# Kernel optimization log

Hardware: AMD Instinct MI355X
Metric: run time of the kernel (lower is better)

## Reference

```python
import jax, jax.numpy as jnp
import numpy as np

N = 50000      # nodes
E = 1_600_000  # edges (avg degree 32)
INP, HID, OUT = 256, 512, 256
N_REST = 11    # GCNConv layers beyond the first (12 total)
BN_EPS = 1e-5


def setup_inputs() -> dict:
    key = jax.random.key(0)
    ks = jax.random.split(key, 8)
    s = 0.05
    return {
        "x": jax.random.normal(ks[0], (N, INP), jnp.float32),
        "edge_index": jax.random.randint(ks[1], (2, E), 0, N, dtype=jnp.int64),
        "W_first": jax.random.normal(ks[2], (INP, HID), jnp.float32) * s,
        "b_first": jnp.zeros((HID,), jnp.float32),
        "W_rest": jax.random.normal(ks[3], (N_REST, HID, HID), jnp.float32) * s,
        "b_rest": jnp.zeros((N_REST, HID), jnp.float32),
        "bn_gamma": jnp.ones((2, HID), jnp.float32),
        "bn_beta": jnp.zeros((2, HID), jnp.float32),
        "out_W": jax.random.normal(ks[4], (HID, OUT), jnp.float32) * s,
        "out_b": jnp.zeros((OUT,), jnp.float32),
    }


def _gelu(v):
    return jax.nn.gelu(v, approximate=False)  # nn.GELU default (erf)


def reference(x, edge_index, W_first, b_first, W_rest, b_rest,
              bn_gamma, bn_beta, out_W, out_b):
    n = x.shape[0]
    # GCN normalization with self-loops: A_hat = D^-1/2 (A + I) D^-1/2
    loops = jnp.arange(n, dtype=edge_index.dtype)
    row = jnp.concatenate([edge_index[0], loops])  # source
    col = jnp.concatenate([edge_index[1], loops])  # target
    deg = jax.ops.segment_sum(jnp.ones_like(col, x.dtype), col, num_segments=n)
    dinv = jnp.where(deg > 0, jax.lax.rsqrt(deg), 0.0)
    norm = dinv[row] * dinv[col]  # [E+N]

    def conv(h, W, b):
        msg = (h @ W)[row] * norm[:, None]                      # gather + scale
        return jax.ops.segment_sum(msg, col, num_segments=n) + b  # scatter-add

    def bn(h, g, bta):  # BatchNorm1d, training-mode batch stats
        mu = h.mean(0)
        var = h.var(0)
        return (h - mu) * jax.lax.rsqrt(var + BN_EPS) * g + bta

    # block 0: conv, gelu, conv, gelu, conv (pyg BasicGNN: no act after last)
    h = conv(x, W_first, b_first)
    h = conv(_gelu(h), W_rest[0], b_rest[0])
    h = conv(_gelu(h), W_rest[1], b_rest[1])
    wi = 2
    for blk in range(3):
        h = conv(h, W_rest[wi], b_rest[wi])
        h = conv(_gelu(h), W_rest[wi + 1], b_rest[wi + 1])
        h = conv(_gelu(h), W_rest[wi + 2], b_rest[wi + 2])
        wi += 3
        if blk != 2:
            h = _gelu(bn(h, bn_gamma[blk], bn_beta[blk]))
    return h @ out_W + out_b
```

## Files before the change

### kernel.cpp

```cpp
#include <hip/hip_runtime.h>
#include <hip/hip_fp16.h>
#include <math.h>

#define INP 256
#define HID 512
#define OUTD 256

typedef _Float16 f16x8 __attribute__((ext_vector_type(8)));
typedef float f32x4 __attribute__((ext_vector_type(4)));

__device__ __forceinline__ float gelu_f(float x) {
  return 0.5f * x * (1.0f + erff(x * 0.7071067811865475f));
}

__device__ __forceinline__ void fma4(float4& a, float w, const float4& x) {
  a.x = fmaf(w, x.x, a.x);
  a.y = fmaf(w, x.y, a.y);
  a.z = fmaf(w, x.z, a.z);
  a.w = fmaf(w, x.w, a.w);
}

__device__ __forceinline__ void fma8h(float4& a0, float4& a1, float w,
                                      const float4& rv) {
  const __half2* h = (const __half2*)&rv;
  float2 f0 = __half22float2(h[0]);
  float2 f1 = __half22float2(h[1]);
  float2 f2 = __half22float2(h[2]);
  float2 f3 = __half22float2(h[3]);
  a0.x = fmaf(w, f0.x, a0.x); a0.y = fmaf(w, f0.y, a0.y);
  a0.z = fmaf(w, f1.x, a0.z); a0.w = fmaf(w, f1.y, a0.w);
  a1.x = fmaf(w, f2.x, a1.x); a1.y = fmaf(w, f2.y, a1.y);
  a1.z = fmaf(w, f3.x, a1.z); a1.w = fmaf(w, f3.y, a1.w);
}


__global__ void hist_k(const int* __restrict__ col, int* __restrict__ cnt, int E) {
  int e = blockIdx.x * blockDim.x + threadIdx.x;
  if (e < E) atomicAdd(&cnt[col[e]], 1);
}

__global__ void dinv_k(const int* __restrict__ cnt, float* __restrict__ dinv, int n) {
  int i = blockIdx.x * blockDim.x + threadIdx.x;
  if (i < n) dinv[i] = rsqrtf((float)(cnt[i] + 1));
}

__global__ void scan1_k(const int* __restrict__ cnt, int* __restrict__ offs,
                        int* __restrict__ bsum, int n) {
  __shared__ int s[256];
  int t = threadIdx.x;
  int i = blockIdx.x * 256 + t;
  int v = (i < n) ? cnt[i] : 0;
  s[t] = v;
  __syncthreads();
  #pragma unroll
  for (int off = 1; off < 256; off <<= 1) {
    int u = (t >= off) ? s[t - off] : 0;
    __syncthreads();
    s[t] += u;
    __syncthreads();
  }
  if (i < n) offs[i] = s[t] - v;
  if (t == 255) bsum[blockIdx.x] = s[255];
}

__global__ void scan2_k(int* __restrict__ bsum, int nb) {
  __shared__ int s[256];
  int t = threadIdx.x;
  int v = (t < nb) ? bsum[t] : 0;
  s[t] = v;
  __syncthreads();
  #pragma unroll
  for (int off = 1; off < 256; off <<= 1) {
    int u = (t >= off) ? s[t - off] : 0;
    __syncthreads();
    s[t] += u;
    __syncthreads();
  }
  if (t < nb) bsum[t] = s[t] - v;
}

__global__ void scan3_k(int* __restrict__ offs, const int* __restrict__ bsum, int n) {
  int i = blockIdx.x * 256 + threadIdx.x;
  if (i < n) offs[i] += bsum[blockIdx.x];
}

__global__ void scatter_k(const int* __restrict__ row, const int* __restrict__ col,
                          const int* __restrict__ offs, int* __restrict__ cur,
                          const float* __restrict__ dinv, int* __restrict__ srcs,
                          float* __restrict__ norms, int E) {
  int e = blockIdx.x * blockDim.x + threadIdx.x;
  if (e >= E) return;
  int r = row[e], c = col[e];
  int p = offs[c] + atomicAdd(&cur[c], 1);
  srcs[p] = r;
  norms[p] = dinv[r] * dinv[c];
}

template <int PRO, int BIAS, int HALFC>
__global__ __launch_bounds__(256) void gemm_k(
    const float* __restrict__ A, const float* __restrict__ B, void* __restrict__ Cv,
    int M, int K, int NN, const float* __restrict__ bias,
    const float* __restrict__ scale, const float* __restrict__ shift) {
  __shared__ f16x8 Asl[4][128];
  __shared__ f16x8 Bsl[4][128];
  const int t = threadIdx.x;
  const int l = t & 63, wid = t >> 6;
  const int lid = l & 15, cc = l >> 4;
  const int wr = wid >> 1, wc = wid & 1;
  const int bm = blockIdx.x * 128, bn = blockIdx.y * 128;

  const int aq = t & 3;
  const int am = t >> 2;
  const int bc = t >> 6;
  const int bn0 = t & 63;

  f32x4 acc[4][4];
  #pragma unroll
  for (int i = 0; i < 4; ++i)
    #pragma unroll
    for (int j = 0; j < 4; ++j) acc[i][j] = (f32x4)0.f;

  for (int k0 = 0; k0 < K; k0 += 32) {
    #pragma unroll
    for (int h = 0; h < 2; ++h) {
      const int m = am + h * 64;
      const int gm = bm + m;
      const int gk = k0 + aq * 8;
      float4 v0 = make_float4(0.f, 0.f, 0.f, 0.f), v1 = v0;
      if (gm < M) {
        v0 = *(const float4*)(A + (size_t)gm * K + gk);
        v1 = *(const float4*)(A + (size_t)gm * K + gk + 4);
      }
      if (PRO == 2) {
        const float4 s0 = *(const float4*)(scale + gk);
        const float4 s1 = *(const float4*)(scale + gk + 4);
        const float4 h0 = *(const float4*)(shift + gk);
        const float4 h1 = *(const float4*)(shift + gk + 4);
        v0.x = fmaf(v0.x, s0.x, h0.x); v0.y = fmaf(v0.y, s0.y, h0.y);
        v0.z = fmaf(v0.z, s0.z, h0.z); v0.w = fmaf(v0.w, s0.w, h0.w);
        v1.x = fmaf(v1.x, s1.x, h1.x); v1.y = fmaf(v1.y, s1.y, h1.y);
        v1.z = fmaf(v1.z, s1.z, h1.z); v1.w = fmaf(v1.w, s1.w, h1.w);
      }
      if (PRO >= 1) {
        v0.x = gelu_f(v0.x); v0.y = gelu_f(v0.y);
        v0.z = gelu_f(v0.z); v0.w = gelu_f(v0.w);
        v1.x = gelu_f(v1.x); v1.y = gelu_f(v1.y);
        v1.z = gelu_f(v1.z); v1.w = gelu_f(v1.w);
      }
      f16x8 hv;
      hv[0] = (_Float16)v0.x; hv[1] = (_Float16)v0.y;
      hv[2] = (_Float16)v0.z; hv[3] = (_Float16)v0.w;
      hv[4] = (_Float16)v1.x; hv[5] = (_Float16)v1.y;
      hv[6] = (_Float16)v1.z; hv[7] = (_Float16)v1.w;
      Asl[aq][m] = hv;
    }
    #pragma unroll
    for (int h = 0; h < 2; ++h) {
      const int nn = bn0 + h * 64;
      f16x8 hv;
      #pragma unroll
      for (int j = 0; j < 8; ++j)
        hv[j] = (_Float16)B[(size_t)(k0 + bc * 8 + j) * NN + bn + nn];
      Bsl[bc][nn] = hv;
    }
    __syncthreads();
    f16x8 af[4], bf[4];
    #pragma unroll
    for (int i = 0; i < 4; ++i) af[i] = Asl[cc][wr * 64 + i * 16 + lid];
    #pragma unroll
    for (int j = 0; j < 4; ++j) bf[j] = Bsl[cc][wc * 64 + j * 16 + lid];
    #pragma unroll
    for (int i = 0; i < 4; ++i)
      #pragma unroll
      for (int j = 0; j < 4; ++j)
        acc[i][j] = __builtin_amdgcn_mfma_f32_16x16x32_f16(af[i], bf[j],
                                                           acc[i][j], 0, 0, 0);
    __syncthreads();
  }

  #pragma unroll
  for (int j = 0; j < 4; ++j) {
    const int col = bn + wc * 64 + j * 16 + lid;
    const float bv = BIAS ? bias[col] : 0.f;
    #pragma unroll
    for (int i = 0; i < 4; ++i) {
      #pragma unroll
      for (int r = 0; r < 4; ++r) {
        const int row = bm + wr * 64 + i * 16 + cc * 4 + r;
        if (row < M) {
          const float o = acc[i][j][r] + bv;
          if (HALFC)
            ((__half*)Cv)[(size_t)row * NN + col] = __float2half(o);
          else
            ((float*)Cv)[(size_t)row * NN + col] = o;
        }
      }
    }
  }
}

template <int D>
__global__ __launch_bounds__(256) void agg_k(
    const float* __restrict__ xw, const int* __restrict__ srcs,
    const float* __restrict__ norms, const int* __restrict__ offs,
    const int* __restrict__ cnt, const float* __restrict__ dinv,
    const float* __restrict__ bias, float* __restrict__ out, int n) {
  constexpr int NV = D / 256;
  int wid = (blockIdx.x * blockDim.x + threadIdx.x) >> 6;
  int lane = threadIdx.x & 63;
  if (wid >= n) return;
  const int base = offs[wid];
  const int num = cnt[wid];

  float4 acc[NV];
  #pragma unroll
  for (int v = 0; v < NV; ++v) acc[v] = make_float4(0.f, 0.f, 0.f, 0.f);

  int sA[4], sB[4];
  float wA[4], wB[4];
  float4 rA[4][NV], rB[4][NV];

  auto ldidx = [&](int e, int& s, float& w) {
    bool ok = e < num;
    s = ok ? srcs[base + e] : 0;
    w = ok ? norms[base + e] : 0.f;
  };

  const int nw = (num + 3) >> 2;

  if (nw > 0) {
    #pragma unroll
    for (int j = 0; j < 4; ++j) ldidx(j, sA[j], wA[j]);
    #pragma unroll
    for (int j = 0; j < 4; ++j) {
      const float4* rp = (const float4*)(xw + (size_t)sA[j] * D);
      #pragma unroll
      for (int v = 0; v < NV; ++v) rA[j][v] = rp[v * 64 + lane];
    }
    int w = 0;
    for (; w + 2 <= nw; w += 2) {
      #pragma unroll
      for (int j = 0; j < 4; ++j) ldidx((w + 1) * 4 + j, sB[j], wB[j]);
      #pragma unroll
      for (int j = 0; j < 4; ++j) {
        const float4* rp = (const float4*)(xw + (size_t)sB[j] * D);
        #pragma unroll
        for (int v = 0; v < NV; ++v) rB[j][v] = rp[v * 64 + lane];
      }
      #pragma unroll
      for (int j = 0; j < 4; ++j)
        #pragma unroll
        for (int v = 0; v < NV; ++v) fma4(acc[v], wA[j], rA[j][v]);
      if (w + 2 < nw) {
        #pragma unroll
        for (int j = 0; j < 4; ++j) ldidx((w + 2) * 4 + j, sA[j], wA[j]);
        #pragma unroll
        for (int j = 0; j < 4; ++j) {
          const float4* rp = (const float4*)(xw + (size_t)sA[j] * D);
          #pragma unroll
          for (int v = 0; v < NV; ++v) rA[j][v] = rp[v * 64 + lane];
        }
      }
      #pragma unroll
      for (int j = 0; j < 4; ++j)
        #pragma unroll
        for (int v = 0; v < NV; ++v) fma4(acc[v], wB[j], rB[j][v]);
    }
    if (w < nw) {
      #pragma unroll
      for (int j = 0; j < 4; ++j)
        #pragma unroll
        for (int v = 0; v < NV; ++v) fma4(acc[v], wA[j], rA[j][v]);
    }
  }

  {
    float di = dinv[wid];
    float ws = di * di;
    const float4* rs = (const float4*)(xw + (size_t)wid * D);
    #pragma unroll
    for (int v = 0; v < NV; ++v) {
      float4 xs = rs[v * 64 + lane];
      fma4(acc[v], ws, xs);
    }
  }
  if (bias) {
    #pragma unroll
    for (int v = 0; v < NV; ++v) {
      float4 b = ((const float4*)bias)[v * 64 + lane];
      acc[v].x += b.x; acc[v].y += b.y; acc[v].z += b.z; acc[v].w += b.w;
    }
  }
  float4* op = (float4*)(out + (size_t)wid * D);
  #pragma unroll
  for (int v = 0; v < NV; ++v) op[v * 64 + lane] = acc[v];
}

__global__ __launch_bounds__(256) void agg_h_k(
    const __half* __restrict__ xwh, const int* __restrict__ srcs,
    const float* __restrict__ norms, const int* __restrict__ offs,
    const int* __restrict__ cnt, const float* __restrict__ dinv,
    const float* __restrict__ bias, float* __restrict__ out, int n) {
  int wid = (blockIdx.x * blockDim.x + threadIdx.x) >> 6;
  int lane = threadIdx.x & 63;
  if (wid >= n) return;
  const int base = offs[wid];
  const int num = cnt[wid];

  float4 a0 = make_float4(0.f, 0.f, 0.f, 0.f);
  float4 a1 = make_float4(0.f, 0.f, 0.f, 0.f);

  int sA[4], sB[4];
  float wA[4], wB[4];
  float4 rA[4], rB[4];

  auto ldidx = [&](int e, int& s, float& w) {
    bool ok = e < num;
    s = ok ? srcs[base + e] : 0;
    w = ok ? norms[base + e] : 0.f;
  };

  const int nw = (num + 3) >> 2;

  if (nw > 0) {
    #pragma unroll
    for (int j = 0; j < 4; ++j) ldidx(j, sA[j], wA[j]);
    #pragma unroll
    for (int j = 0; j < 4; ++j)
      rA[j] = ((const float4*)(xwh + (size_t)sA[j] * HID))[lane];
    int w = 0;
    for (; w + 2 <= nw; w += 2) {
      #pragma unroll
      for (int j = 0; j < 4; ++j) ldidx((w + 1) * 4 + j, sB[j], wB[j]);
      #pragma unroll
      for (int j = 0; j < 4; ++j)
        rB[j] = ((const float4*)(xwh + (size_t)sB[j] * HID))[lane];
      #pragma unroll
      for (int j = 0; j < 4; ++j) fma8h(a0, a1, wA[j], rA[j]);
      if (w + 2 < nw) {
        #pragma unroll
        for (int j = 0; j < 4; ++j) ldidx((w + 2) * 4 + j, sA[j], wA[j]);
        #pragma unroll
        for (int j = 0; j < 4; ++j)
          rA[j] = ((const float4*)(xwh + (size_t)sA[j] * HID))[lane];
      }
      #pragma unroll
      for (int j = 0; j < 4; ++j) fma8h(a0, a1, wB[j], rB[j]);
    }
    if (w < nw) {
      #pragma unroll
      for (int j = 0; j < 4; ++j) fma8h(a0, a1, wA[j], rA[j]);
    }
  }

  {
    float di = dinv[wid];
    float ws = di * di;
    float4 rs = ((const float4*)(xwh + (size_t)wid * HID))[lane];
    fma8h(a0, a1, ws, rs);
  }
  const float4 b0 = *(const float4*)(bias + lane * 8);
  const float4 b1 = *(const float4*)(bias + lane * 8 + 4);
  a0.x += b0.x; a0.y += b0.y; a0.z += b0.z; a0.w += b0.w;
  a1.x += b1.x; a1.y += b1.y; a1.z += b1.z; a1.w += b1.w;
  float* op = out + (size_t)wid * HID + lane * 8;
  *(float4*)op = a0;
  *(float4*)(op + 4) = a1;
}

__global__ __launch_bounds__(512) void bn_stats_k(const float* __restrict__ F,
                                                  float* __restrict__ sums, int n) {
  int t = threadIdx.x;
  int r0 = blockIdx.x * 128;
  int r1 = min(r0 + 128, n);
  float s = 0.f, s2 = 0.f;
  for (int r = r0; r < r1; ++r) {
    float v = F[(size_t)r * HID + t];
    s += v;
    s2 = fmaf(v, v, s2);
  }
  atomicAdd(&sums[t], s);
  atomicAdd(&sums[HID + t], s2);
}

__global__ void bn_fin_k(const float* __restrict__ sums, const float* __restrict__ g,
                         const float* __restrict__ b, float* __restrict__ scale,
                         float* __restrict__ shift, int n) {
  int t = threadIdx.x;
  float inv = 1.0f / (float)n;
  float mu = sums[t] * inv;
  float var = fmaf(-mu, mu, sums[HID + t] * inv);
  float rs = rsqrtf(var + 1e-5f);
  float sc = g[t] * rs;
  scale[t] = sc;
  shift[t] = fmaf(-mu, sc, b[t]);
}

extern "C" void kernel_launch(void* const* d_in, const int* in_sizes, int n_in,
                              void* d_out, int out_size, void* d_ws, size_t ws_size,
                              hipStream_t stream) {
  const float* x     = (const float*)d_in[0];
  const int*   ei    = (const int*)d_in[1];
  const float* Wf    = (const float*)d_in[2];
  const float* bf    = (const float*)d_in[3];
  const float* Wr    = (const float*)d_in[4];
  const float* br    = (const float*)d_in[5];
  const float* gamma = (const float*)d_in[6];
  const float* beta  = (const float*)d_in[7];
  const float* Wo    = (const float*)d_in[8];
  const float* bo    = (const float*)d_in[9];
  float* out = (float*)d_out;

  const int n = in_sizes[0] / INP;
  const int E = in_sizes[1] / 2;
  const int* erow = ei;
  const int* ecol = ei + E;

  char* w = (char*)d_ws;
  float*  f0   = (float*)w;  w += (size_t)n * HID * sizeof(float);
  __half* xwh  = (__half*)w; w += (size_t)n * HID * sizeof(__half);
  float*  t256 = (float*)w;  w += (size_t)n * INP * sizeof(float);

  char* q = (char*)d_out;
  int*   srcs  = (int*)q;   q += (size_t)E * sizeof(int);
  float* norms = (float*)q; q += (size_t)E * sizeof(float);
  int*   cnt   = (int*)q;   q += (size_t)n * sizeof(int);
  int*   cur   = (int*)q;   q += (size_t)n * sizeof(int);
  int*   offs  = (int*)q;   q += (size_t)n * sizeof(int);
  int*   bsum  = (int*)q;   q += 256 * sizeof(int);
  float* dinv  = (float*)q; q += (size_t)n * sizeof(float);
  float* bnsum = (float*)q; q += 1024 * sizeof(float);
  float* bnsc  = (float*)q; q += 512 * sizeof(float);
  float* bnsh  = (float*)q; q += 512 * sizeof(float);

  hipMemsetAsync(cnt, 0, (size_t)n * sizeof(int), stream);
  hipMemsetAsync(cur, 0, (size_t)n * sizeof(int), stream);

  const int eb = (E + 255) / 256;
  const int nb = (n + 255) / 256;
  hist_k<<<eb, 256, 0, stream>>>(ecol, cnt, E);
  dinv_k<<<nb, 256, 0, stream>>>(cnt, dinv, n);
  scan1_k<<<nb, 256, 0, stream>>>(cnt, offs, bsum, n);
  scan2_k<<<1, 256, 0, stream>>>(bsum, nb);
  scan3_k<<<nb, 256, 0, stream>>>(offs, bsum, n);
  scatter_k<<<eb, 256, 0, stream>>>(erow, ecol, offs, cur, dinv, srcs, norms, E);

  const dim3 blk(256);
  const int mg = (n + 127) / 128;
  const dim3 g512(mg, HID / 128);
  const dim3 g256(mg, OUTD / 128);
  const int aggBlocks = (n + 3) / 4;

  auto conv = [&](const float* W, const float* b, int pro) {
    if (pro == 1)
      gemm_k<1, 0, 1><<<g512, blk, 0, stream>>>(f0, W, xwh, n, HID, HID, nullptr, nullptr, nullptr);
    else if (pro == 2)
      gemm_k<2, 0, 1><<<g512, blk, 0, stream>>>(f0, W, xwh, n, HID, HID, nullptr, bnsc, bnsh);
    else
      gemm_k<0, 0, 1><<<g512, blk, 0, stream>>>(f0, W, xwh, n, HID, HID, nullptr, nullptr, nullptr);
    agg_h_k<<<aggBlocks, blk, 0, stream>>>(xwh, srcs, norms, offs, cnt, dinv, b, f0, n);
  };
  auto bn = [&](const float* F, int g) {
    hipMemsetAsync(bnsum, 0, 1024 * sizeof(float), stream);
    bn_stats_k<<<(n + 127) / 128, 512, 0, stream>>>(F, bnsum, n);
    bn_fin_k<<<1, 512, 0, stream>>>(bnsum, gamma + (size_t)g * HID,
                                    beta + (size_t)g * HID, bnsc, bnsh, n);
  };
  const size_t WS = (size_t)HID * HID;

  agg_k<INP><<<aggBlocks, blk, 0, stream>>>(x, srcs, norms, offs, cnt, dinv,
                                            nullptr, t256, n);
  gemm_k<0, 1, 0><<<g512, blk, 0, stream>>>(t256, Wf, f0, n, INP, HID, bf, nullptr, nullptr);

  conv(Wr + 0 * WS,  br + 0 * HID,  1);
  conv(Wr + 1 * WS,  br + 1 * HID,  1);
  conv(Wr + 2 * WS,  br + 2 * HID,  0);
  conv(Wr + 3 * WS,  br + 3 * HID,  1);
  conv(Wr + 4 * WS,  br + 4 * HID,  1);
  bn(f0, 0);
  conv(Wr + 5 * WS,  br + 5 * HID,  2);
  conv(Wr + 6 * WS,  br + 6 * HID,  1);
  conv(Wr + 7 * WS,  br + 7 * HID,  1);
  bn(f0, 1);
  conv(Wr + 8 * WS,  br + 8 * HID,  2);
  conv(Wr + 9 * WS,  br + 9 * HID,  1);
  conv(Wr + 10 * WS, br + 10 * HID, 1);
  gemm_k<0, 1, 0><<<g256, blk, 0, stream>>>(f0, Wo, out, n, HID, OUTD, bo, nullptr, nullptr);
}
```

Baseline: 4.550 ms.

## Store inter-layer activations in fp16 and move GELU into producer epilogues

Activations between layers are now stored as fp16 instead of fp32. The input x is cast to fp16 up front, the first aggregation reads fp16 rows, and GELU is applied once in the aggregation or GEMM epilogue rather than in every GEMM tile's prologue. This roughly halves the bytes moved by GEMM A-loads, aggregation writes and BN stats, and stops GELU being recomputed for each column tile. In exchange it adds a cast kernel and extra fp16 rounding of activations, and BN statistics are computed from fp16 values.

```diff
diff --git a/kernel.cpp b/kernel.cpp
--- a/kernel.cpp
+++ b/kernel.cpp
@@ -7,17 +7,11 @@
 #define OUTD 256
 
 typedef _Float16 f16x8 __attribute__((ext_vector_type(8)));
+typedef _Float16 f16x4 __attribute__((ext_vector_type(4)));
 typedef float f32x4 __attribute__((ext_vector_type(4)));
 
 __device__ __forceinline__ float gelu_f(float x) {
   return 0.5f * x * (1.0f + erff(x * 0.7071067811865475f));
-}
-
-__device__ __forceinline__ void fma4(float4& a, float w, const float4& x) {
-  a.x = fmaf(w, x.x, a.x);
-  a.y = fmaf(w, x.y, a.y);
-  a.z = fmaf(w, x.z, a.z);
-  a.w = fmaf(w, x.w, a.w);
 }
 
 __device__ __forceinline__ void fma8h(float4& a0, float4& a1, float w,
@@ -33,6 +27,29 @@
   a1.z = fmaf(w, f3.x, a1.z); a1.w = fmaf(w, f3.y, a1.w);
 }
 
+__device__ __forceinline__ void fma4h(float4& a, float w, const float2& rv) {
+  const __half2* h = (const __half2*)&rv;
+  float2 f0 = __half22float2(h[0]);
+  float2 f1 = __half22float2(h[1]);
+  a.x = fmaf(w, f0.x, a.x); a.y = fmaf(w, f0.y, a.y);
+  a.z = fmaf(w, f1.x, a.z); a.w = fmaf(w, f1.y, a.w);
+}
+
+
+__global__ void cast16_k(const float* __restrict__ in, __half* __restrict__ o,
+                         int nElem) {
+  int i = (blockIdx.x * blockDim.x + threadIdx.x) * 8;
+  if (i >= nElem) return;
+  float4 v0 = *(const float4*)(in + i);
+  float4 v1 = *(const float4*)(in + i + 4);
+  f16x8 hv;
+  hv[0] = (_Float16)v0.x; hv[1] = (_Float16)v0.y;
+  hv[2] = (_Float16)v0.z; hv[3] = (_Float16)v0.w;
+  hv[4] = (_Float16)v1.x; hv[5] = (_Float16)v1.y;
+  hv[6] = (_Float16)v1.z; hv[7] = (_Float16)v1.w;
+  *(f16x8*)(o + i) = hv;
+}
+
 
 __global__ void hist_k(const int* __restrict__ col, int* __restrict__ cnt, int E) {
   int e = blockIdx.x * blockDim.x + threadIdx.x;
@@ -96,9 +113,9 @@
   norms[p] = dinv[r] * dinv[c];
 }
 
-template <int PRO, int BIAS, int HALFC>
+template <int PRO, int BIAS, int HALFC, int EPI>
 __global__ __launch_bounds__(256) void gemm_k(
-    const float* __restrict__ A, const float* __restrict__ B, void* __restrict__ Cv,
+    const __half* __restrict__ A, const float* __restrict__ B, void* __restrict__ Cv,
     int M, int K, int NN, const float* __restrict__ bias,
     const float* __restrict__ scale, const float* __restrict__ shift) {
   __shared__ f16x8 Asl[4][128];
@@ -126,32 +143,23 @@
       const int m = am + h * 64;
       const int gm = bm + m;
       const int gk = k0 + aq * 8;
-      float4 v0 = make_float4(0.f, 0.f, 0.f, 0.f), v1 = v0;
-      if (gm < M) {
-        v0 = *(const float4*)(A + (size_t)gm * K + gk);
-        v1 = *(const float4*)(A + (size_t)gm * K + gk + 4);
-      }
+      f16x8 hv;
+      if (gm < M) hv = *(const f16x8*)(A + (size_t)gm * K + gk);
+      else hv = (f16x8)(_Float16)0;
       if (PRO == 2) {
         const float4 s0 = *(const float4*)(scale + gk);
         const float4 s1 = *(const float4*)(scale + gk + 4);
         const float4 h0 = *(const float4*)(shift + gk);
         const float4 h1 = *(const float4*)(shift + gk + 4);
-        v0.x = fmaf(v0.x, s0.x, h0.x); v0.y = fmaf(v0.y, s0.y, h0.y);
-        v0.z = fmaf(v0.z, s0.z, h0.z); v0.w = fmaf(v0.w, s0.w, h0.w);
-        v1.x = fmaf(v1.x, s1.x, h1.x); v1.y = fmaf(v1.y, s1.y, h1.y);
-        v1.z = fmaf(v1.z, s1.z, h1.z); v1.w = fmaf(v1.w, s1.w, h1.w);
+        const float sc[8] = {s0.x, s0.y, s0.z, s0.w, s1.x, s1.y, s1.z, s1.w};
+        const float sh[8] = {h0.x, h0.y, h0.z, h0.w, h1.x, h1.y, h1.z, h1.w};
+        #pragma unroll
+        for (int j = 0; j < 8; ++j) {
+          float v = (float)hv[j];
+          v = gelu_f(fmaf(v, sc[j], sh[j]));
+          hv[j] = (_Float16)v;
+        }
       }
-      if (PRO >= 1) {
-        v0.x = gelu_f(v0.x); v0.y = gelu_f(v0.y);
-        v0.z = gelu_f(v0.z); v0.w = gelu_f(v0.w);
-        v1.x = gelu_f(v1.x); v1.y = gelu_f(v1.y);
-        v1.z = gelu_f(v1.z); v1.w = gelu_f(v1.w);
-      }
-      f16x8 hv;
-      hv[0] = (_Float16)v0.x; hv[1] = (_Float16)v0.y;
-      hv[2] = (_Float16)v0.z; hv[3] = (_Float16)v0.w;
-      hv[4] = (_Float16)v1.x; hv[5] = (_Float16)v1.y;
-      hv[6] = (_Float16)v1.z; hv[7] = (_Float16)v1.w;
       Asl[aq][m] = hv;
     }
     #pragma unroll
@@ -188,7 +196,8 @@
       for (int r = 0; r < 4; ++r) {
         const int row = bm + wr * 64 + i * 16 + cc * 4 + r;
         if (row < M) {
-          const float o = acc[i][j][r] + bv;
+          float o = acc[i][j][r] + bv;
+          if (EPI) o = gelu_f(o);
           if (HALFC)
             ((__half*)Cv)[(size_t)row * NN + col] = __float2half(o);
           else
@@ -199,108 +208,12 @@
   }
 }
 
-template <int D>
-__global__ __launch_bounds__(256) void agg_k(
-    const float* __restrict__ xw, const int* __restrict__ srcs,
-    const float* __restrict__ norms, const int* __restrict__ offs,
-    const int* __restrict__ cnt, const float* __restrict__ dinv,
-    const float* __restrict__ bias, float* __restrict__ out, int n) {
-  constexpr int NV = D / 256;
-  int wid = (blockIdx.x * blockDim.x + threadIdx.x) >> 6;
-  int lane = threadIdx.x & 63;
-  if (wid >= n) return;
-  const int base = offs[wid];
-  const int num = cnt[wid];
-
-  float4 acc[NV];
-  #pragma unroll
-  for (int v = 0; v < NV; ++v) acc[v] = make_float4(0.f, 0.f, 0.f, 0.f);
-
-  int sA[4], sB[4];
-  float wA[4], wB[4];
-  float4 rA[4][NV], rB[4][NV];
-
-  auto ldidx = [&](int e, int& s, float& w) {
-    bool ok = e < num;
-    s = ok ? srcs[base + e] : 0;
-    w = ok ? norms[base + e] : 0.f;
-  };
-
-  const int nw = (num + 3) >> 2;
-
-  if (nw > 0) {
-    #pragma unroll
-    for (int j = 0; j < 4; ++j) ldidx(j, sA[j], wA[j]);
-    #pragma unroll
-    for (int j = 0; j < 4; ++j) {
-      const float4* rp = (const float4*)(xw + (size_t)sA[j] * D);
-      #pragma unroll
-      for (int v = 0; v < NV; ++v) rA[j][v] = rp[v * 64 + lane];
-    }
-    int w = 0;
-    for (; w + 2 <= nw; w += 2) {
-      #pragma unroll
-      for (int j = 0; j < 4; ++j) ldidx((w + 1) * 4 + j, sB[j], wB[j]);
-      #pragma unroll
-      for (int j = 0; j < 4; ++j) {
-        const float4* rp = (const float4*)(xw + (size_t)sB[j] * D);
-        #pragma unroll
-        for (int v = 0; v < NV; ++v) rB[j][v] = rp[v * 64 + lane];
-      }
-      #pragma unroll
-      for (int j = 0; j < 4; ++j)
-        #pragma unroll
-        for (int v = 0; v < NV; ++v) fma4(acc[v], wA[j], rA[j][v]);
-      if (w + 2 < nw) {
-        #pragma unroll
-        for (int j = 0; j < 4; ++j) ldidx((w + 2) * 4 + j, sA[j], wA[j]);
-        #pragma unroll
-        for (int j = 0; j < 4; ++j) {
-          const float4* rp = (const float4*)(xw + (size_t)sA[j] * D);
-          #pragma unroll
-          for (int v = 0; v < NV; ++v) rA[j][v] = rp[v * 64 + lane];
-        }
-      }
-      #pragma unroll
-      for (int j = 0; j < 4; ++j)
-        #pragma unroll
-        for (int v = 0; v < NV; ++v) fma4(acc[v], wB[j], rB[j][v]);
-    }
-    if (w < nw) {
-      #pragma unroll
-      for (int j = 0; j < 4; ++j)
-        #pragma unroll
-        for (int v = 0; v < NV; ++v) fma4(acc[v], wA[j], rA[j][v]);
-    }
-  }
-
-  {
-    float di = dinv[wid];
-    float ws = di * di;
-    const float4* rs = (const float4*)(xw + (size_t)wid * D);
-    #pragma unroll
-    for (int v = 0; v < NV; ++v) {
-      float4 xs = rs[v * 64 + lane];
-      fma4(acc[v], ws, xs);
-    }
-  }
-  if (bias) {
-    #pragma unroll
-    for (int v = 0; v < NV; ++v) {
-      float4 b = ((const float4*)bias)[v * 64 + lane];
-      acc[v].x += b.x; acc[v].y += b.y; acc[v].z += b.z; acc[v].w += b.w;
-    }
-  }
-  float4* op = (float4*)(out + (size_t)wid * D);
-  #pragma unroll
-  for (int v = 0; v < NV; ++v) op[v * 64 + lane] = acc[v];
-}
-
-__global__ __launch_bounds__(256) void agg_h_k(
+template <int EPI>
+__global__ __launch_bounds__(256) void agg512_k(
     const __half* __restrict__ xwh, const int* __restrict__ srcs,
     const float* __restrict__ norms, const int* __restrict__ offs,
     const int* __restrict__ cnt, const float* __restrict__ dinv,
-    const float* __restrict__ bias, float* __restrict__ out, int n) {
+    const float* __restrict__ bias, __half* __restrict__ out, int n) {
   int wid = (blockIdx.x * blockDim.x + threadIdx.x) >> 6;
   int lane = threadIdx.x & 63;
   if (wid >= n) return;
@@ -361,21 +274,93 @@
   }
   const float4 b0 = *(const float4*)(bias + lane * 8);
   const float4 b1 = *(const float4*)(bias + lane * 8 + 4);
-  a0.x += b0.x; a0.y += b0.y; a0.z += b0.z; a0.w += b0.w;
-  a1.x += b1.x; a1.y += b1.y; a1.z += b1.z; a1.w += b1.w;
-  float* op = out + (size_t)wid * HID + lane * 8;
-  *(float4*)op = a0;
-  *(float4*)(op + 4) = a1;
-}
-
-__global__ __launch_bounds__(512) void bn_stats_k(const float* __restrict__ F,
-                                                  float* __restrict__ sums, int n) {
+  float o[8] = {a0.x + b0.x, a0.y + b0.y, a0.z + b0.z, a0.w + b0.w,
+                a1.x + b1.x, a1.y + b1.y, a1.z + b1.z, a1.w + b1.w};
+  f16x8 hv;
+  #pragma unroll
+  for (int j = 0; j < 8; ++j) {
+    float v = EPI ? gelu_f(o[j]) : o[j];
+    hv[j] = (_Float16)v;
+  }
+  *(f16x8*)(out + (size_t)wid * HID + lane * 8) = hv;
+}
+
+__global__ __launch_bounds__(256) void agg256_k(
+    const __half* __restrict__ x16, const int* __restrict__ srcs,
+    const float* __restrict__ norms, const int* __restrict__ offs,
+    const int* __restrict__ cnt, const float* __restrict__ dinv,
+    __half* __restrict__ out, int n) {
+  int wid = (blockIdx.x * blockDim.x + threadIdx.x) >> 6;
+  int lane = threadIdx.x & 63;
+  if (wid >= n) return;
+  const int base = offs[wid];
+  const int num = cnt[wid];
+
+  float4 a0 = make_float4(0.f, 0.f, 0.f, 0.f);
+
+  int sA[4], sB[4];
+  float wA[4], wB[4];
+  float2 rA[4], rB[4];
+
+  auto ldidx = [&](int e, int& s, float& w) {
+    bool ok = e < num;
+    s = ok ? srcs[base + e] : 0;
+    w = ok ? norms[base + e] : 0.f;
+  };
+
+  const int nw = (num + 3) >> 2;
+
+  if (nw > 0) {
+    #pragma unroll
+    for (int j = 0; j < 4; ++j) ldidx(j, sA[j], wA[j]);
+    #pragma unroll
+    for (int j = 0; j < 4; ++j)
+      rA[j] = ((const float2*)(x16 + (size_t)sA[j] * INP))[lane];
+    int w = 0;
+    for (; w + 2 <= nw; w += 2) {
+      #pragma unroll
+      for (int j = 0; j < 4; ++j) ldidx((w + 1) * 4 + j, sB[j], wB[j]);
+      #pragma unroll
+      for (int j = 0; j < 4; ++j)
+        rB[j] = ((const float2*)(x16 + (size_t)sB[j] * INP))[lane];
+      #pragma unroll
+      for (int j = 0; j < 4; ++j) fma4h(a0, wA[j], rA[j]);
+      if (w + 2 < nw) {
+        #pragma unroll
+        for (int j = 0; j < 4; ++j) ldidx((w + 2) * 4 + j, sA[j], wA[j]);
+        #pragma unroll
+        for (int j = 0; j < 4; ++j)
+          rA[j] = ((const float2*)(x16 + (size_t)sA[j] * INP))[lane];
+      }
+      #pragma unroll
+      for (int j = 0; j < 4; ++j) fma4h(a0, wB[j], rB[j]);
+    }
+    if (w < nw) {
+      #pragma unroll
+      for (int j = 0; j < 4; ++j) fma4h(a0, wA[j], rA[j]);
+    }
+  }
+
+  {
+    float di = dinv[wid];
+    float ws = di * di;
+    float2 rs = ((const float2*)(x16 + (size_t)wid * INP))[lane];
+    fma4h(a0, ws, rs);
+  }
+  f16x4 hv;
+  hv[0] = (_Float16)a0.x; hv[1] = (_Float16)a0.y;
+  hv[2] = (_Float16)a0.z; hv[3] = (_Float16)a0.w;
+  *(f16x4*)(out + (size_t)wid * INP + lane * 4) = hv;
+}
+
+__global__ __launch_bounds__(512) void bn_stats_h_k(const __half* __restrict__ F,
+                                                    float* __restrict__ sums, int n) {
   int t = threadIdx.x;
   int r0 = blockIdx.x * 128;
   int r1 = min(r0 + 128, n);
   float s = 0.f, s2 = 0.f;
   for (int r = r0; r < r1; ++r) {
-    float v = F[(size_t)r * HID + t];
+    float v = __half2float(F[(size_t)r * HID + t]);
     s += v;
     s2 = fmaf(v, v, s2);
   }
@@ -417,9 +402,10 @@
   const int* ecol = ei + E;
 
   char* w = (char*)d_ws;
-  float*  f0   = (float*)w;  w += (size_t)n * HID * sizeof(float);
-  __half* xwh  = (__half*)w; w += (size_t)n * HID * sizeof(__half);
-  float*  t256 = (float*)w;  w += (size_t)n * INP * sizeof(float);
+  __half* a16   = (__half*)w; w += (size_t)n * HID * sizeof(__half);
+  __half* xwh   = (__half*)w; w += (size_t)n * HID * sizeof(__half);
+  __half* x16   = (__half*)w; w += (size_t)n * INP * sizeof(__half);
+  __half* t256h = (__half*)w; w += (size_t)n * INP * sizeof(__half);
 
   char* q = (char*)d_out;
   int*   srcs  = (int*)q;   q += (size_t)E * sizeof(int);
@@ -438,6 +424,7 @@
 
   const int eb = (E + 255) / 256;
   const int nb = (n + 255) / 256;
+  cast16_k<<<(n * INP / 8 + 255) / 256, 256, 0, stream>>>(x, x16, n * INP);
   hist_k<<<eb, 256, 0, stream>>>(ecol, cnt, E);
   dinv_k<<<nb, 256, 0, stream>>>(cnt, dinv, n);
   scan1_k<<<nb, 256, 0, stream>>>(cnt, offs, bsum, n);
@@ -451,39 +438,40 @@
   const dim3 g256(mg, OUTD / 128);
   const int aggBlocks = (n + 3) / 4;
 
-  auto conv = [&](const float* W, const float* b, int pro) {
-    if (pro == 1)
-      gemm_k<1, 0, 1><<<g512, blk, 0, stream>>>(f0, W, xwh, n, HID, HID, nullptr, nullptr, nullptr);
-    else if (pro == 2)
-      gemm_k<2, 0, 1><<<g512, blk, 0, stream>>>(f0, W, xwh, n, HID, HID, nullptr, bnsc, bnsh);
+  auto conv = [&](const float* W, const float* b, int pro, int epi) {
+    if (pro == 2)
+      gemm_k<2, 0, 1, 0><<<g512, blk, 0, stream>>>(a16, W, xwh, n, HID, HID, nullptr, bnsc, bnsh);
     else
-      gemm_k<0, 0, 1><<<g512, blk, 0, stream>>>(f0, W, xwh, n, HID, HID, nullptr, nullptr, nullptr);
-    agg_h_k<<<aggBlocks, blk, 0, stream>>>(xwh, srcs, norms, offs, cnt, dinv, b, f0, n);
+      gemm_k<0, 0, 1, 0><<<g512, blk, 0, stream>>>(a16, W, xwh, n, HID, HID, nullptr, nullptr, nullptr);
+    if (epi)
+      agg512_k<1><<<aggBlocks, blk, 0, stream>>>(xwh, srcs, norms, offs, cnt, dinv, b, a16, n);
+    else
+      agg512_k<0><<<aggBlocks, blk, 0, stream>>>(xwh, srcs, norms, offs, cnt, dinv, b, a16, n);
   };
-  auto bn = [&](const float* F, int g) {
+  auto bn = [&](int g) {
     hipMemsetAsync(bnsum, 0, 1024 * sizeof(float), stream);
-    bn_stats_k<<<(n + 127) / 128, 512, 0, stream>>>(F, bnsum, n);
+    bn_stats_h_k<<<(n + 127) / 128, 512, 0, stream>>>(a16, bnsum, n);
     bn_fin_k<<<1, 512, 0, stream>>>(bnsum, gamma + (size_t)g * HID,
                                     beta + (size_t)g * HID, bnsc, bnsh, n);
   };
   const size_t WS = (size_t)HID * HID;
 
-  agg_k<INP><<<aggBlocks, blk, 0, stream>>>(x, srcs, norms, offs, cnt, dinv,
-                                            nullptr, t256, n);
-  gemm_k<0, 1, 0><<<g512, blk, 0, stream>>>(t256, Wf, f0, n, INP, HID, bf, nullptr, nullptr);
-
-  conv(Wr + 0 * WS,  br + 0 * HID,  1);
-  conv(Wr + 1 * WS,  br + 1 * HID,  1);
-  conv(Wr + 2 * WS,  br + 2 * HID,  0);
-  conv(Wr + 3 * WS,  br + 3 * HID,  1);
-  conv(Wr + 4 * WS,  br + 4 * HID,  1);
-  bn(f0, 0);
-  conv(Wr + 5 * WS,  br + 5 * HID,  2);
-  conv(Wr + 6 * WS,  br + 6 * HID,  1);
-  conv(Wr + 7 * WS,  br + 7 * HID,  1);
-  bn(f0, 1);
-  conv(Wr + 8 * WS,  br + 8 * HID,  2);
-  conv(Wr + 9 * WS,  br + 9 * HID,  1);
-  conv(Wr + 10 * WS, br + 10 * HID, 1);
-  gemm_k<0, 1, 0><<<g256, blk, 0, stream>>>(f0, Wo, out, n, HID, OUTD, bo, nullptr, nullptr);
-}
+  agg256_k<<<aggBlocks, blk, 0, stream>>>(x16, srcs, norms, offs, cnt, dinv,
+                                          t256h, n);
+  gemm_k<0, 1, 1, 1><<<g512, blk, 0, stream>>>(t256h, Wf, a16, n, INP, HID, bf, nullptr, nullptr);
+
+  conv(Wr + 0 * WS,  br + 0 * HID,  0, 1);
+  conv(Wr + 1 * WS,  br + 1 * HID,  0, 0);
+  conv(Wr + 2 * WS,  br + 2 * HID,  0, 1);
+  conv(Wr + 3 * WS,  br + 3 * HID,  0, 1);
+  conv(Wr + 4 * WS,  br + 4 * HID,  0, 0);
+  bn(0);
+  conv(Wr + 5 * WS,  br + 5 * HID,  2, 1);
+  conv(Wr + 6 * WS,  br + 6 * HID,  0, 1);
+  conv(Wr + 7 * WS,  br + 7 * HID,  0, 0);
+  bn(1);
+  conv(Wr + 8 * WS,  br + 8 * HID,  2, 1);
+  conv(Wr + 9 * WS,  br + 9 * HID,  0, 1);
+  conv(Wr + 10 * WS, br + 10 * HID, 0, 0);
+  gemm_k<0, 1, 0, 0><<<g256, blk, 0, stream>>>(a16, Wo, out, n, HID, OUTD, bo, nullptr, nullptr);
+}
```

Measured after the change: 3.936 ms. 13.5% less time.
